# Kernel tuning notes

Hardware: AMD Instinct MI355X
Metric: run time of the kernel (lower is better)

Reference implementation:

```python
import jax, jax.numpy as jnp
import numpy as np

B, T, D = 64, 512, 1024
V_TAG, V_TYPE = 6, 20
TAG_PAD, TYPE_PAD = 5, 19
E = 2048          # total entity spans in the batch (sliced cascade mode)
MAX_SPAN = 8      # max entity span length


def setup_inputs() -> dict:
    key = jax.random.key(0)
    ks = jax.random.split(key, 12)
    full_hidden = jax.random.normal(ks[0], (B, T, D), dtype=jnp.float32)
    W_tag = jax.random.normal(ks[1], (D, V_TAG), dtype=jnp.float32) * 0.02
    b_tag = jnp.zeros((V_TAG,), jnp.float32)
    W_type = jax.random.normal(ks[2], (D, V_TYPE), dtype=jnp.float32) * 0.02
    b_type = jnp.zeros((V_TYPE,), jnp.float32)
    crf_start = jax.random.normal(ks[3], (V_TAG,), dtype=jnp.float32) * 0.1
    crf_end = jax.random.normal(ks[4], (V_TAG,), dtype=jnp.float32) * 0.1
    crf_trans = jax.random.normal(ks[5], (V_TAG, V_TAG), dtype=jnp.float32) * 0.1
    # ragged sequence lengths (>= MAX_SPAN+1 so all positions/spans are sane)
    seq_lens = jnp.maximum(jax.random.randint(ks[6], (B,), 1, T + 1), MAX_SPAN + 1).astype(jnp.int32)
    tag_ids = jax.random.randint(ks[7], (B, T), 0, V_TAG - 1).astype(jnp.int32)  # exclude pad tag
    ent_sample_ids = jax.random.randint(ks[8], (E,), 0, B).astype(jnp.int32)
    ent_starts = jax.random.randint(ks[9], (E,), 0, T - MAX_SPAN).astype(jnp.int32)
    ent_lens = jax.random.randint(ks[10], (E,), 1, MAX_SPAN + 1)
    ent_ends = (ent_starts + ent_lens).astype(jnp.int32)
    ent_type_ids = jax.random.randint(ks[11], (E,), 0, V_TYPE - 1).astype(jnp.int32)  # exclude pad type
    return dict(full_hidden=full_hidden, W_tag=W_tag, b_tag=b_tag, W_type=W_type,
                b_type=b_type, crf_start=crf_start, crf_end=crf_end, crf_trans=crf_trans,
                tag_ids=tag_ids, seq_lens=seq_lens, ent_sample_ids=ent_sample_ids,
                ent_starts=ent_starts, ent_ends=ent_ends, ent_type_ids=ent_type_ids)


def reference(full_hidden, W_tag, b_tag, W_type, b_type, crf_start, crf_end, crf_trans,
              tag_ids, seq_lens, ent_sample_ids, ent_starts, ent_ends, ent_type_ids):
    mask = jnp.arange(T)[None, :] < seq_lens[:, None]                  # [B,T] bool (tok_mask)
    maskf = mask.astype(full_hidden.dtype)

    # ---- base CRF decoder: tag projection + CRF NLL per sample ----
    tag_feats = full_hidden @ W_tag + b_tag                            # [B,T,V_TAG]

    # gold path score
    emit_scores = jnp.take_along_axis(tag_feats, tag_ids[..., None].astype(jnp.int32), axis=-1)[..., 0]  # [B,T]
    gold = crf_start[tag_ids[:, 0]] + jnp.sum(emit_scores * maskf, axis=1)
    trans_scores = crf_trans[tag_ids[:, :-1], tag_ids[:, 1:]]          # [B,T-1]
    gold = gold + jnp.sum(trans_scores * maskf[:, 1:], axis=1)
    last_tags = tag_ids[jnp.arange(B), seq_lens - 1]
    gold = gold + crf_end[last_tags]

    # log-partition via forward algorithm (log-sum-exp DP, lax.scan over time)
    alpha0 = crf_start[None, :] + tag_feats[:, 0]                      # [B,V]

    def step(alpha, xs):
        emit_t, mask_t = xs                                            # [B,V], [B]
        new = jax.scipy.special.logsumexp(
            alpha[:, :, None] + crf_trans[None, :, :] + emit_t[:, None, :], axis=1)
        return jnp.where(mask_t[:, None], new, alpha), None

    alphaT, _ = jax.lax.scan(step, alpha0,
                             (jnp.swapaxes(tag_feats, 0, 1)[1:], mask.T[1:]))
    logZ = jax.scipy.special.logsumexp(alphaT + crf_end[None, :], axis=-1)  # [B]
    tag_losses = logZ - gold                                           # per-sample CRF NLL

    # ---- sliced cascade: entity-span mean pooling + CE(sum) per sample ----
    type_feats = full_hidden @ W_type + b_type                         # [B,T,V_TYPE]
    csum = jnp.pad(jnp.cumsum(type_feats, axis=1), ((0, 0), (1, 0), (0, 0)))  # [B,T+1,V_TYPE]
    span_sum = csum[ent_sample_ids, ent_ends] - csum[ent_sample_ids, ent_starts]  # [E,V_TYPE]
    span_len = (ent_ends - ent_starts).astype(type_feats.dtype)
    ent_feats = span_sum / span_len[:, None]                           # mean over span
    logp = jax.nn.log_softmax(ent_feats, axis=-1)
    ent_ce = -jnp.take_along_axis(logp, ent_type_ids[:, None].astype(jnp.int32), axis=-1)[:, 0]
    valid = (ent_type_ids != TYPE_PAD).astype(ent_ce.dtype)            # ignore_index
    type_losses = jax.ops.segment_sum(ent_ce * valid, ent_sample_ids, num_segments=B)
    return tag_losses + type_losses                                    # [B]
```

## Files before the change

### kernel.cpp

```cpp
#include <hip/hip_runtime.h>
#include <math.h>
#include <stdint.h>

#define NB  64
#define NT  512
#define ND  1024
#define NVT 6
#define NVY 20
#define TYPE_PAD_V 19
#define NE  2048
#define LOG2E 1.44269504088896340736f
#define LN2   0.69314718055994530942f

typedef float v2f __attribute__((ext_vector_type(2)));

__global__ __launch_bounds__(256) void k1_tagfeats(const float* __restrict__ H,
                                                   const float* __restrict__ W_tag,
                                                   const float* __restrict__ b_tag,
                                                   float* __restrict__ featsT,
                                                   float* __restrict__ featsE) {
    __shared__ float wlds[NVT][ND];
    for (int i = threadIdx.x; i < ND * NVT; i += 256) {
        int d = i / NVT, v = i % NVT;
        wlds[v][d] = W_tag[i];
    }
    __syncthreads();
    float bt[NVT];
#pragma unroll
    for (int v = 0; v < NVT; ++v) bt[v] = b_tag[v];

    const int lane = threadIdx.x & 63;
    const int wid  = threadIdx.x >> 6;
    const int qw   = lane >> 4;
    const int ql   = lane & 15;
    const int rowBase = blockIdx.x * 32;

#pragma unroll
    for (int it = 0; it < 2; ++it) {
        const int r = rowBase + it * 16 + wid * 4 + qw;
        const float4* hrow = (const float4*)(H + (size_t)r * ND);
        float acc[NVT] = {0.f, 0.f, 0.f, 0.f, 0.f, 0.f};
#pragma unroll
        for (int k = 0; k < 16; ++k) {
            float4 h = hrow[ql + 16 * k];
#pragma unroll
            for (int v = 0; v < NVT; ++v) {
                float4 w = ((const float4*)&wlds[v][0])[ql + 16 * k];
                acc[v] += h.x * w.x + h.y * w.y + h.z * w.z + h.w * w.w;
            }
        }
#pragma unroll
        for (int v = 0; v < NVT; ++v) {
#pragma unroll
            for (int off = 8; off >= 1; off >>= 1)
                acc[v] += __shfl_xor(acc[v], off);
        }
        const int bb = r >> 9;
        const int tt = r & (NT - 1);
#pragma unroll
        for (int v = 0; v < NVT; ++v)
            if (ql == v) {
                float val = acc[v] + bt[v];
                featsT[(size_t)tt * 384 + bb * 6 + v] = val;
                featsE[(size_t)tt * 512 + bb * 6 + 2 * (bb >> 4) + v] =
                    __builtin_amdgcn_exp2f(val * LOG2E);
            }
    }
}

__global__ __launch_bounds__(64) void k2a_chunks(
    const float* __restrict__ featsE,
    const float* __restrict__ crf_trans,
    const int* __restrict__ seq_lens,
    const float* __restrict__ W_type,
    float* __restrict__ WtT,
    float* __restrict__ out,
    float* __restrict__ ws2) {
    const int c = blockIdx.x / 6;
    const int k = blockIdx.x - 6 * c;
    const int b = threadIdx.x;
    if (blockIdx.x == 0) out[b] = 0.0f;
    {
        int tid = blockIdx.x * 64 + b;
        for (int i = tid; i < NVY * ND; i += 192 * 64)
            WtT[i] = W_type[(i & (ND - 1)) * NVY + (i >> 10)];
    }
    const int L = seq_lens[b];
    float F[NVT][NVT];
#pragma unroll
    for (int i = 0; i < NVT; ++i)
#pragma unroll
        for (int j = 0; j < NVT; ++j)
            F[i][j] = __builtin_amdgcn_exp2f(crf_trans[i * NVT + j] * LOG2E);
    const char* pl = (const char*)featsE + b * 24 + (b >> 4) * 8;
    v2f Ebuf[16][3];
#pragma unroll
    for (int u = 0; u < 16; ++u) {
        const v2f* p = (const v2f*)(pl + (size_t)(16 * c + 1 + u) * 2048);
        Ebuf[u][0] = p[0]; Ebuf[u][1] = p[1]; Ebuf[u][2] = p[2];
    }
    float v0, v1, v2, v3, v4, v5;
    v0 = (k == 0) ? 1.f : 0.f; v1 = (k == 1) ? 1.f : 0.f; v2 = (k == 2) ? 1.f : 0.f;
    v3 = (k == 3) ? 1.f : 0.f; v4 = (k == 4) ? 1.f : 0.f; v5 = (k == 5) ? 1.f : 0.f;
    int isc = 0;
#pragma unroll
    for (int u = 0; u < 16; ++u) {
        float e0 = Ebuf[u][0].x, e1 = Ebuf[u][0].y, e2 = Ebuf[u][1].x,
              e3 = Ebuf[u][1].y, e4 = Ebuf[u][2].x, e5 = Ebuf[u][2].y;
        bool ok = (16 * c + 1 + u) < L;
        float g[NVT];
#pragma unroll
        for (int j = 0; j < NVT; ++j) {
            float s = F[0][j] * v0;
            s = __builtin_fmaf(F[1][j], v1, s);
            s = __builtin_fmaf(F[2][j], v2, s);
            s = __builtin_fmaf(F[3][j], v3, s);
            s = __builtin_fmaf(F[4][j], v4, s);
            s = __builtin_fmaf(F[5][j], v5, s);
            g[j] = s;
        }
        v0 = ok ? e0 * g[0] : v0;  v1 = ok ? e1 * g[1] : v1;
        v2 = ok ? e2 * g[2] : v2;  v3 = ok ? e3 * g[3] : v3;
        v4 = ok ? e4 * g[4] : v4;  v5 = ok ? e5 * g[5] : v5;
        if ((u & 3) == 3) {
            float qmax = fmaxf(fmaxf(fmaxf(v0, v1), v2), fmaxf(fmaxf(v3, v4), v5));
            uint32_t eb = __float_as_uint(qmax) >> 23;
            float ri = __uint_as_float((uint32_t)(253 - eb) << 23);
            v0 *= ri; v1 *= ri; v2 *= ri; v3 *= ri; v4 *= ri; v5 *= ri;
            isc += (int)eb - 126;
        }
    }
    float4* dst = (float4*)(ws2 + (((size_t)c * 6 + k) * 64 + b) * 8);
    dst[0] = make_float4(v0, v1, v2, v3);
    dst[1] = make_float4(v4, v5, (float)isc, 0.0f);
}

#define LOADC(BUF, c) do {                                                   \
    _Pragma("unroll")                                                        \
    for (int kk = 0; kk < 6; ++kk) {                                         \
        const float4* p = src4 + (size_t)((c) * 6 + kk) * 128;               \
        BUF[2 * kk] = p[0]; BUF[2 * kk + 1] = p[1];                          \
    }                                                                        \
} while (0)

#define CBODY(BUF, c) do {                                                   \
    float i0 = BUF[1].z, i1 = BUF[3].z, i2 = BUF[5].z,                       \
          i3 = BUF[7].z, i4 = BUF[9].z, i5 = BUF[11].z;                      \
    float im = fmaxf(fmaxf(fmaxf(i0, i1), i2), fmaxf(fmaxf(i3, i4), i5));    \
    float w0 = q0 * __builtin_amdgcn_exp2f(i0 - im);                         \
    float w1 = q1 * __builtin_amdgcn_exp2f(i1 - im);                         \
    float w2 = q2 * __builtin_amdgcn_exp2f(i2 - im);                         \
    float w3 = q3 * __builtin_amdgcn_exp2f(i3 - im);                         \
    float w4 = q4 * __builtin_amdgcn_exp2f(i4 - im);                         \
    float w5 = q5 * __builtin_amdgcn_exp2f(i5 - im);                         \
    float n0 = BUF[0].x * w0, n1 = BUF[0].y * w0, n2 = BUF[0].z * w0,        \
          n3 = BUF[0].w * w0, n4 = BUF[1].x * w0, n5 = BUF[1].y * w0;        \
    n0 = __builtin_fmaf(BUF[2].x,  w1, n0); n1 = __builtin_fmaf(BUF[2].y,  w1, n1); \
    n2 = __builtin_fmaf(BUF[2].z,  w1, n2); n3 = __builtin_fmaf(BUF[2].w,  w1, n3); \
    n4 = __builtin_fmaf(BUF[3].x,  w1, n4); n5 = __builtin_fmaf(BUF[3].y,  w1, n5); \
    n0 = __builtin_fmaf(BUF[4].x,  w2, n0); n1 = __builtin_fmaf(BUF[4].y,  w2, n1); \
    n2 = __builtin_fmaf(BUF[4].z,  w2, n2); n3 = __builtin_fmaf(BUF[4].w,  w2, n3); \
    n4 = __builtin_fmaf(BUF[5].x,  w2, n4); n5 = __builtin_fmaf(BUF[5].y,  w2, n5); \
    n0 = __builtin_fmaf(BUF[6].x,  w3, n0); n1 = __builtin_fmaf(BUF[6].y,  w3, n1); \
    n2 = __builtin_fmaf(BUF[6].z,  w3, n2); n3 = __builtin_fmaf(BUF[6].w,  w3, n3); \
    n4 = __builtin_fmaf(BUF[7].x,  w3, n4); n5 = __builtin_fmaf(BUF[7].y,  w3, n5); \
    n0 = __builtin_fmaf(BUF[8].x,  w4, n0); n1 = __builtin_fmaf(BUF[8].y,  w4, n1); \
    n2 = __builtin_fmaf(BUF[8].z,  w4, n2); n3 = __builtin_fmaf(BUF[8].w,  w4, n3); \
    n4 = __builtin_fmaf(BUF[9].x,  w4, n4); n5 = __builtin_fmaf(BUF[9].y,  w4, n5); \
    n0 = __builtin_fmaf(BUF[10].x, w5, n0); n1 = __builtin_fmaf(BUF[10].y, w5, n1); \
    n2 = __builtin_fmaf(BUF[10].z, w5, n2); n3 = __builtin_fmaf(BUF[10].w, w5, n3); \
    n4 = __builtin_fmaf(BUF[11].x, w5, n4); n5 = __builtin_fmaf(BUF[11].y, w5, n5); \
    float qmax = fmaxf(fmaxf(fmaxf(n0, n1), n2), fmaxf(fmaxf(n3, n4), n5));  \
    uint32_t eb = __float_as_uint(qmax) >> 23;                               \
    mAcc2 += (float)((int)eb - 126) + im;                                    \
    float ri = __uint_as_float((uint32_t)(253 - eb) << 23);                  \
    q0 = n0 * ri; q1 = n1 * ri; q2 = n2 * ri;                                \
    q3 = n3 * ri; q4 = n4 * ri; q5 = n5 * ri;                                \
    int lc = (c) + 3; if (lc > 31) lc = 31;                                  \
    LOADC(BUF, lc);                                                          \
} while (0)

__global__ __launch_bounds__(64) void k2_fused(
    const float* __restrict__ featsT,
    const float* __restrict__ ws2,
    const float* __restrict__ WtT,
    const float* __restrict__ H,
    const float* __restrict__ b_type,
    const float* __restrict__ crf_start,
    const float* __restrict__ crf_end,
    const float* __restrict__ crf_trans,
    const int* __restrict__ tag_ids,
    const int* __restrict__ seq_lens,
    const int* __restrict__ ent_sid,
    const int* __restrict__ ent_st,
    const int* __restrict__ ent_en,
    const int* __restrict__ ent_ty,
    float* __restrict__ out) {
    __shared__ int stag[NT];
    __shared__ float trLp[NVT * NVT];
    const int lane = threadIdx.x;

    if (blockIdx.x == 0) {
        const int b = lane;
        float a0[NVT];
#pragma unroll
        for (int j = 0; j < NVT; ++j) a0[j] = crf_start[j] + featsT[b * 6 + j];
        float m0 = fmaxf(fmaxf(fmaxf(a0[0], a0[1]), a0[2]),
                         fmaxf(fmaxf(a0[3], a0[4]), a0[5]));
        float q0 = __builtin_amdgcn_exp2f((a0[0] - m0) * LOG2E);
        float q1 = __builtin_amdgcn_exp2f((a0[1] - m0) * LOG2E);
        float q2 = __builtin_amdgcn_exp2f((a0[2] - m0) * LOG2E);
        float q3 = __builtin_amdgcn_exp2f((a0[3] - m0) * LOG2E);
        float q4 = __builtin_amdgcn_exp2f((a0[4] - m0) * LOG2E);
        float q5 = __builtin_amdgcn_exp2f((a0[5] - m0) * LOG2E);
        float mAcc2 = m0 * LOG2E;

        const float4* src4 = (const float4*)ws2 + b * 2;
        float4 PB0[12], PB1[12], PB2[12];
        LOADC(PB0, 0); LOADC(PB1, 1); LOADC(PB2, 2);
#pragma unroll 1
        for (int c0 = 0; c0 < 30; c0 += 3) {
            CBODY(PB0, c0);
            CBODY(PB1, c0 + 1);
            CBODY(PB2, c0 + 2);
        }
        CBODY(PB0, 30);
        CBODY(PB1, 31);

        float fe0 = __builtin_amdgcn_exp2f(crf_end[0] * LOG2E);
        float fe1 = __builtin_amdgcn_exp2f(crf_end[1] * LOG2E);
        float fe2 = __builtin_amdgcn_exp2f(crf_end[2] * LOG2E);
        float fe3 = __builtin_amdgcn_exp2f(crf_end[3] * LOG2E);
        float fe4 = __builtin_amdgcn_exp2f(crf_end[4] * LOG2E);
        float fe5 = __builtin_amdgcn_exp2f(crf_end[5] * LOG2E);
        float zs = q0 * fe0 + q1 * fe1 + q2 * fe2 + q3 * fe3 + q4 * fe4 + q5 * fe5;
        float logZ = LN2 * (mAcc2 + __builtin_amdgcn_logf(zs));
        atomicAdd(&out[b], logZ);
    } else if (blockIdx.x <= NB) {
        const int b = blockIdx.x - 1;
        for (int i = lane; i < NT; i += 64) stag[i] = tag_ids[b * NT + i];
        if (lane < NVT * NVT) trLp[lane] = crf_trans[lane];
        __syncthreads();
        const int L = seq_lens[b];
        float g = 0.0f;
#pragma unroll
        for (int k = 0; k < NT / 64; ++k) {
            int t = lane + 64 * k;
            if (t < L) {
                int tg = stag[t];
                g += featsT[(size_t)t * 384 + b * 6 + tg];
                if (t >= 1) g += trLp[stag[t - 1] * NVT + tg];
            }
        }
#pragma unroll
        for (int off = 32; off >= 1; off >>= 1) g += __shfl_xor(g, off);
        if (lane == 0)
            atomicAdd(&out[b], -(g + crf_start[stag[0]] + crf_end[stag[L - 1]]));
    } else {
        const int e  = blockIdx.x - NB - 1;
        const int bb = ent_sid[e];
        const int s  = ent_st[e];
        const int en = ent_en[e];
        const int ty = ent_ty[e];
        float4 sv[4];
#pragma unroll
        for (int k = 0; k < 4; ++k) { sv[k].x = 0.f; sv[k].y = 0.f; sv[k].z = 0.f; sv[k].w = 0.f; }
        for (int t = s; t < en; ++t) {
            const float4* hr = (const float4*)(H + ((size_t)bb * NT + t) * ND);
#pragma unroll
            for (int k = 0; k < 4; ++k) {
                float4 h = hr[lane + 64 * k];
                sv[k].x += h.x; sv[k].y += h.y; sv[k].z += h.z; sv[k].w += h.w;
            }
        }
        const float inv = 1.0f / (float)(en - s);
        float f[NVY];
#pragma unroll
        for (int v = 0; v < NVY; ++v) {
            const float4* wv = (const float4*)(WtT + v * ND);
            float p = 0.0f;
#pragma unroll
            for (int k = 0; k < 4; ++k) {
                float4 w = wv[lane + 64 * k];
                p += sv[k].x * w.x + sv[k].y * w.y + sv[k].z * w.z + sv[k].w * w.w;
            }
#pragma unroll
            for (int off = 32; off >= 1; off >>= 1) p += __shfl_xor(p, off);
            f[v] = p * inv + b_type[v];
        }
        float mx = -3.0e38f;
#pragma unroll
        for (int v = 0; v < NVY; ++v) mx = fmaxf(mx, f[v]);
        float sum = 0.0f, goldf = 0.0f;
#pragma unroll
        for (int v = 0; v < NVY; ++v) {
            sum += __expf(f[v] - mx);
            if (v == ty) goldf = f[v];
        }
        float lse = mx + __logf(sum);
        if (ty != TYPE_PAD_V && lane == 0) atomicAdd(&out[bb], lse - goldf);
    }
}

extern "C" void kernel_launch(void* const* d_in, const int* in_sizes, int n_in,
                              void* d_out, int out_size, void* d_ws, size_t ws_size,
                              hipStream_t stream) {
    const float* H         = (const float*)d_in[0];
    const float* W_tag     = (const float*)d_in[1];
    const float* b_tag     = (const float*)d_in[2];
    const float* W_type    = (const float*)d_in[3];
    const float* b_type    = (const float*)d_in[4];
    const float* crf_start = (const float*)d_in[5];
    const float* crf_end   = (const float*)d_in[6];
    const float* crf_trans = (const float*)d_in[7];
    const int* tag_ids     = (const int*)d_in[8];
    const int* seq_lens    = (const int*)d_in[9];
    const int* ent_sid     = (const int*)d_in[10];
    const int* ent_st      = (const int*)d_in[11];
    const int* ent_en      = (const int*)d_in[12];
    const int* ent_ty      = (const int*)d_in[13];
    float* out = (float*)d_out;
    float* ws  = (float*)d_ws;
    float* featsE = ws;
    float* featsT = ws + 262144;
    float* WtT    = ws + 262144 + 196608;
    float* ws2    = ws + 262144 + 196608 + 20480;

    hipLaunchKernelGGL(k1_tagfeats, dim3(1024), dim3(256), 0, stream,
                       H, W_tag, b_tag, featsT, featsE);
    hipLaunchKernelGGL(k2a_chunks, dim3(192), dim3(64), 0, stream,
                       featsE, crf_trans, seq_lens, W_type, WtT, out, ws2);
    hipLaunchKernelGGL(k2_fused, dim3(1 + NB + NE), dim3(64), 0, stream,
                       featsT, ws2, WtT, H, b_type, crf_start, crf_end, crf_trans,
                       tag_ids, seq_lens, ent_sid, ent_st, ent_en, ent_ty, out);
}
```

Measured before the change: 62.77 us.

## Fold CRF chunk kernel into fused kernel with last-block combine via atomic counter

Removes the separate chunk-scan kernel. Its 192 blocks now run inside the fused kernel, and the last block to finish, found through an atomic counter and threadfence, performs the sequential chunk combine for logZ. The W_type transpose and output zeroing move into the tag-projection kernel, and the separate exp feature buffer is dropped, with exponentials recomputed from featsT in the chunk blocks. This saves one launch and lets the CRF combine overlap with the span-pooling blocks, but the combine now waits on the slowest chunk block, and the recomputed exponentials add work.

```diff
diff --git a/kernel.cpp b/kernel.cpp
--- a/kernel.cpp
+++ b/kernel.cpp
@@ -14,11 +14,28 @@
 
 typedef float v2f __attribute__((ext_vector_type(2)));
 
+#define OFF_WTT 196608
+#define OFF_CNT 217088
+#define OFF_WS2 217104
+
 __global__ __launch_bounds__(256) void k1_tagfeats(const float* __restrict__ H,
                                                    const float* __restrict__ W_tag,
                                                    const float* __restrict__ b_tag,
-                                                   float* __restrict__ featsT,
-                                                   float* __restrict__ featsE) {
+                                                   const float* __restrict__ W_type,
+                                                   float* __restrict__ ws,
+                                                   float* __restrict__ out) {
+    float* featsT = ws;
+    float* WtT    = ws + OFF_WTT;
+    if (blockIdx.x == 0) {
+        if (threadIdx.x < NB) out[threadIdx.x] = 0.0f;
+        if (threadIdx.x == 64) ((int*)(ws + OFF_CNT))[0] = 0;
+    }
+    if (blockIdx.x < 32) {
+        int tid = blockIdx.x * 256 + threadIdx.x;
+        for (int i = tid; i < NVY * ND; i += 32 * 256)
+            WtT[i] = W_type[(i & (ND - 1)) * NVY + (i >> 10)];
+    }
+
     __shared__ float wlds[NVT][ND];
     for (int i = threadIdx.x; i < ND * NVT; i += 256) {
         int d = i / NVT, v = i % NVT;
@@ -59,80 +76,8 @@
         const int tt = r & (NT - 1);
 #pragma unroll
         for (int v = 0; v < NVT; ++v)
-            if (ql == v) {
-                float val = acc[v] + bt[v];
-                featsT[(size_t)tt * 384 + bb * 6 + v] = val;
-                featsE[(size_t)tt * 512 + bb * 6 + 2 * (bb >> 4) + v] =
-                    __builtin_amdgcn_exp2f(val * LOG2E);
-            }
-    }
-}
-
-__global__ __launch_bounds__(64) void k2a_chunks(
-    const float* __restrict__ featsE,
-    const float* __restrict__ crf_trans,
-    const int* __restrict__ seq_lens,
-    const float* __restrict__ W_type,
-    float* __restrict__ WtT,
-    float* __restrict__ out,
-    float* __restrict__ ws2) {
-    const int c = blockIdx.x / 6;
-    const int k = blockIdx.x - 6 * c;
-    const int b = threadIdx.x;
-    if (blockIdx.x == 0) out[b] = 0.0f;
-    {
-        int tid = blockIdx.x * 64 + b;
-        for (int i = tid; i < NVY * ND; i += 192 * 64)
-            WtT[i] = W_type[(i & (ND - 1)) * NVY + (i >> 10)];
-    }
-    const int L = seq_lens[b];
-    float F[NVT][NVT];
-#pragma unroll
-    for (int i = 0; i < NVT; ++i)
-#pragma unroll
-        for (int j = 0; j < NVT; ++j)
-            F[i][j] = __builtin_amdgcn_exp2f(crf_trans[i * NVT + j] * LOG2E);
-    const char* pl = (const char*)featsE + b * 24 + (b >> 4) * 8;
-    v2f Ebuf[16][3];
-#pragma unroll
-    for (int u = 0; u < 16; ++u) {
-        const v2f* p = (const v2f*)(pl + (size_t)(16 * c + 1 + u) * 2048);
-        Ebuf[u][0] = p[0]; Ebuf[u][1] = p[1]; Ebuf[u][2] = p[2];
-    }
-    float v0, v1, v2, v3, v4, v5;
-    v0 = (k == 0) ? 1.f : 0.f; v1 = (k == 1) ? 1.f : 0.f; v2 = (k == 2) ? 1.f : 0.f;
-    v3 = (k == 3) ? 1.f : 0.f; v4 = (k == 4) ? 1.f : 0.f; v5 = (k == 5) ? 1.f : 0.f;
-    int isc = 0;
-#pragma unroll
-    for (int u = 0; u < 16; ++u) {
-        float e0 = Ebuf[u][0].x, e1 = Ebuf[u][0].y, e2 = Ebuf[u][1].x,
-              e3 = Ebuf[u][1].y, e4 = Ebuf[u][2].x, e5 = Ebuf[u][2].y;
-        bool ok = (16 * c + 1 + u) < L;
-        float g[NVT];
-#pragma unroll
-        for (int j = 0; j < NVT; ++j) {
-            float s = F[0][j] * v0;
-            s = __builtin_fmaf(F[1][j], v1, s);
-            s = __builtin_fmaf(F[2][j], v2, s);
-            s = __builtin_fmaf(F[3][j], v3, s);
-            s = __builtin_fmaf(F[4][j], v4, s);
-            s = __builtin_fmaf(F[5][j], v5, s);
-            g[j] = s;
-        }
-        v0 = ok ? e0 * g[0] : v0;  v1 = ok ? e1 * g[1] : v1;
-        v2 = ok ? e2 * g[2] : v2;  v3 = ok ? e3 * g[3] : v3;
-        v4 = ok ? e4 * g[4] : v4;  v5 = ok ? e5 * g[5] : v5;
-        if ((u & 3) == 3) {
-            float qmax = fmaxf(fmaxf(fmaxf(v0, v1), v2), fmaxf(fmaxf(v3, v4), v5));
-            uint32_t eb = __float_as_uint(qmax) >> 23;
-            float ri = __uint_as_float((uint32_t)(253 - eb) << 23);
-            v0 *= ri; v1 *= ri; v2 *= ri; v3 *= ri; v4 *= ri; v5 *= ri;
-            isc += (int)eb - 126;
-        }
-    }
-    float4* dst = (float4*)(ws2 + (((size_t)c * 6 + k) * 64 + b) * 8);
-    dst[0] = make_float4(v0, v1, v2, v3);
-    dst[1] = make_float4(v4, v5, (float)isc, 0.0f);
+            if (ql == v) featsT[(size_t)tt * 384 + bb * 6 + v] = acc[v] + bt[v];
+    }
 }
 
 #define LOADC(BUF, c) do {                                                   \
@@ -181,9 +126,6 @@
 } while (0)
 
 __global__ __launch_bounds__(64) void k2_fused(
-    const float* __restrict__ featsT,
-    const float* __restrict__ ws2,
-    const float* __restrict__ WtT,
     const float* __restrict__ H,
     const float* __restrict__ b_type,
     const float* __restrict__ crf_start,
@@ -195,49 +137,116 @@
     const int* __restrict__ ent_st,
     const int* __restrict__ ent_en,
     const int* __restrict__ ent_ty,
+    float* __restrict__ ws,
     float* __restrict__ out) {
+    const float* featsT = ws;
+    const float* WtT    = ws + OFF_WTT;
+    int* cnt            = (int*)(ws + OFF_CNT);
+    float* ws2          = ws + OFF_WS2;
     __shared__ int stag[NT];
     __shared__ float trLp[NVT * NVT];
+    __shared__ int isLast;
     const int lane = threadIdx.x;
 
-    if (blockIdx.x == 0) {
+    if (blockIdx.x < 192) {
+        const int c = blockIdx.x / 6;
+        const int k = blockIdx.x - 6 * c;
         const int b = lane;
-        float a0[NVT];
-#pragma unroll
-        for (int j = 0; j < NVT; ++j) a0[j] = crf_start[j] + featsT[b * 6 + j];
-        float m0 = fmaxf(fmaxf(fmaxf(a0[0], a0[1]), a0[2]),
-                         fmaxf(fmaxf(a0[3], a0[4]), a0[5]));
-        float q0 = __builtin_amdgcn_exp2f((a0[0] - m0) * LOG2E);
-        float q1 = __builtin_amdgcn_exp2f((a0[1] - m0) * LOG2E);
-        float q2 = __builtin_amdgcn_exp2f((a0[2] - m0) * LOG2E);
-        float q3 = __builtin_amdgcn_exp2f((a0[3] - m0) * LOG2E);
-        float q4 = __builtin_amdgcn_exp2f((a0[4] - m0) * LOG2E);
-        float q5 = __builtin_amdgcn_exp2f((a0[5] - m0) * LOG2E);
-        float mAcc2 = m0 * LOG2E;
-
-        const float4* src4 = (const float4*)ws2 + b * 2;
-        float4 PB0[12], PB1[12], PB2[12];
-        LOADC(PB0, 0); LOADC(PB1, 1); LOADC(PB2, 2);
+        const int L = seq_lens[b];
+        float F[NVT][NVT];
+#pragma unroll
+        for (int i = 0; i < NVT; ++i)
+#pragma unroll
+            for (int j = 0; j < NVT; ++j)
+                F[i][j] = __builtin_amdgcn_exp2f(crf_trans[i * NVT + j] * LOG2E);
+        const char* pf = (const char*)featsT + b * 24;
+        v2f Ebuf[16][3];
+#pragma unroll
+        for (int u = 0; u < 16; ++u) {
+            const v2f* p = (const v2f*)(pf + (size_t)(16 * c + 1 + u) * 1536);
+            Ebuf[u][0] = p[0]; Ebuf[u][1] = p[1]; Ebuf[u][2] = p[2];
+        }
+        float v0, v1, v2, v3, v4, v5;
+        v0 = (k == 0) ? 1.f : 0.f; v1 = (k == 1) ? 1.f : 0.f; v2 = (k == 2) ? 1.f : 0.f;
+        v3 = (k == 3) ? 1.f : 0.f; v4 = (k == 4) ? 1.f : 0.f; v5 = (k == 5) ? 1.f : 0.f;
+        int isc = 0;
+#pragma unroll
+        for (int u = 0; u < 16; ++u) {
+            float e0 = __builtin_amdgcn_exp2f(Ebuf[u][0].x * LOG2E);
+            float e1 = __builtin_amdgcn_exp2f(Ebuf[u][0].y * LOG2E);
+            float e2 = __builtin_amdgcn_exp2f(Ebuf[u][1].x * LOG2E);
+            float e3 = __builtin_amdgcn_exp2f(Ebuf[u][1].y * LOG2E);
+            float e4 = __builtin_amdgcn_exp2f(Ebuf[u][2].x * LOG2E);
+            float e5 = __builtin_amdgcn_exp2f(Ebuf[u][2].y * LOG2E);
+            bool ok = (16 * c + 1 + u) < L;
+            float g[NVT];
+#pragma unroll
+            for (int j = 0; j < NVT; ++j) {
+                float s = F[0][j] * v0;
+                s = __builtin_fmaf(F[1][j], v1, s);
+                s = __builtin_fmaf(F[2][j], v2, s);
+                s = __builtin_fmaf(F[3][j], v3, s);
+                s = __builtin_fmaf(F[4][j], v4, s);
+                s = __builtin_fmaf(F[5][j], v5, s);
+                g[j] = s;
+            }
+            v0 = ok ? e0 * g[0] : v0;  v1 = ok ? e1 * g[1] : v1;
+            v2 = ok ? e2 * g[2] : v2;  v3 = ok ? e3 * g[3] : v3;
+            v4 = ok ? e4 * g[4] : v4;  v5 = ok ? e5 * g[5] : v5;
+            if ((u & 3) == 3) {
+                float qmax = fmaxf(fmaxf(fmaxf(v0, v1), v2), fmaxf(fmaxf(v3, v4), v5));
+                uint32_t eb = __float_as_uint(qmax) >> 23;
+                float ri = __uint_as_float((uint32_t)(253 - eb) << 23);
+                v0 *= ri; v1 *= ri; v2 *= ri; v3 *= ri; v4 *= ri; v5 *= ri;
+                isc += (int)eb - 126;
+            }
+        }
+        float4* dst = (float4*)(ws2 + (((size_t)c * 6 + k) * 64 + b) * 8);
+        dst[0] = make_float4(v0, v1, v2, v3);
+        dst[1] = make_float4(v4, v5, (float)isc, 0.0f);
+
+        __threadfence();
+        if (lane == 0) isLast = (atomicAdd(cnt, 1) == 191);
+        __syncthreads();
+        if (isLast) {
+            __threadfence();
+            const int b2 = lane;
+            float a0[NVT];
+#pragma unroll
+            for (int j = 0; j < NVT; ++j) a0[j] = crf_start[j] + featsT[b2 * 6 + j];
+            float m0 = fmaxf(fmaxf(fmaxf(a0[0], a0[1]), a0[2]),
+                             fmaxf(fmaxf(a0[3], a0[4]), a0[5]));
+            float q0 = __builtin_amdgcn_exp2f((a0[0] - m0) * LOG2E);
+            float q1 = __builtin_amdgcn_exp2f((a0[1] - m0) * LOG2E);
+            float q2 = __builtin_amdgcn_exp2f((a0[2] - m0) * LOG2E);
+            float q3 = __builtin_amdgcn_exp2f((a0[3] - m0) * LOG2E);
+            float q4 = __builtin_amdgcn_exp2f((a0[4] - m0) * LOG2E);
+            float q5 = __builtin_amdgcn_exp2f((a0[5] - m0) * LOG2E);
+            float mAcc2 = m0 * LOG2E;
+
+            const float4* src4 = (const float4*)ws2 + b2 * 2;
+            float4 PB0[12], PB1[12], PB2[12];
+            LOADC(PB0, 0); LOADC(PB1, 1); LOADC(PB2, 2);
 #pragma unroll 1
-        for (int c0 = 0; c0 < 30; c0 += 3) {
-            CBODY(PB0, c0);
-            CBODY(PB1, c0 + 1);
-            CBODY(PB2, c0 + 2);
-        }
-        CBODY(PB0, 30);
-        CBODY(PB1, 31);
-
-        float fe0 = __builtin_amdgcn_exp2f(crf_end[0] * LOG2E);
-        float fe1 = __builtin_amdgcn_exp2f(crf_end[1] * LOG2E);
-        float fe2 = __builtin_amdgcn_exp2f(crf_end[2] * LOG2E);
-        float fe3 = __builtin_amdgcn_exp2f(crf_end[3] * LOG2E);
-        float fe4 = __builtin_amdgcn_exp2f(crf_end[4] * LOG2E);
-        float fe5 = __builtin_amdgcn_exp2f(crf_end[5] * LOG2E);
-        float zs = q0 * fe0 + q1 * fe1 + q2 * fe2 + q3 * fe3 + q4 * fe4 + q5 * fe5;
-        float logZ = LN2 * (mAcc2 + __builtin_amdgcn_logf(zs));
-        atomicAdd(&out[b], logZ);
-    } else if (blockIdx.x <= NB) {
-        const int b = blockIdx.x - 1;
+            for (int c0 = 0; c0 < 30; c0 += 3) {
+                CBODY(PB0, c0);
+                CBODY(PB1, c0 + 1);
+                CBODY(PB2, c0 + 2);
+            }
+            CBODY(PB0, 30);
+            CBODY(PB1, 31);
+
+            float zs = q0 * __builtin_amdgcn_exp2f(crf_end[0] * LOG2E)
+                     + q1 * __builtin_amdgcn_exp2f(crf_end[1] * LOG2E)
+                     + q2 * __builtin_amdgcn_exp2f(crf_end[2] * LOG2E)
+                     + q3 * __builtin_amdgcn_exp2f(crf_end[3] * LOG2E)
+                     + q4 * __builtin_amdgcn_exp2f(crf_end[4] * LOG2E)
+                     + q5 * __builtin_amdgcn_exp2f(crf_end[5] * LOG2E);
+            float logZ = LN2 * (mAcc2 + __builtin_amdgcn_logf(zs));
+            atomicAdd(&out[b2], logZ);
+        }
+    } else if (blockIdx.x < 192 + NB) {
+        const int b = blockIdx.x - 192;
         for (int i = lane; i < NT; i += 64) stag[i] = tag_ids[b * NT + i];
         if (lane < NVT * NVT) trLp[lane] = crf_trans[lane];
         __syncthreads();
@@ -257,7 +266,7 @@
         if (lane == 0)
             atomicAdd(&out[b], -(g + crf_start[stag[0]] + crf_end[stag[L - 1]]));
     } else {
-        const int e  = blockIdx.x - NB - 1;
+        const int e  = blockIdx.x - 192 - NB;
         const int bb = ent_sid[e];
         const int s  = ent_st[e];
         const int en = ent_en[e];
@@ -321,16 +330,10 @@
     const int* ent_ty      = (const int*)d_in[13];
     float* out = (float*)d_out;
     float* ws  = (float*)d_ws;
-    float* featsE = ws;
-    float* featsT = ws + 262144;
-    float* WtT    = ws + 262144 + 196608;
-    float* ws2    = ws + 262144 + 196608 + 20480;
 
     hipLaunchKernelGGL(k1_tagfeats, dim3(1024), dim3(256), 0, stream,
-                       H, W_tag, b_tag, featsT, featsE);
-    hipLaunchKernelGGL(k2a_chunks, dim3(192), dim3(64), 0, stream,
-                       featsE, crf_trans, seq_lens, W_type, WtT, out, ws2);
-    hipLaunchKernelGGL(k2_fused, dim3(1 + NB + NE), dim3(64), 0, stream,
-                       featsT, ws2, WtT, H, b_type, crf_start, crf_end, crf_trans,
-                       tag_ids, seq_lens, ent_sid, ent_st, ent_en, ent_ty, out);
+                       H, W_tag, b_tag, W_type, ws, out);
+    hipLaunchKernelGGL(k2_fused, dim3(192 + NB + NE), dim3(64), 0, stream,
+                       H, b_type, crf_start, crf_end, crf_trans,
+                       tag_ids, seq_lens, ent_sid, ent_st, ent_en, ent_ty, ws, out);
 }
```

Result: faster. 61.44 us (-2.1%).
